# Kernel tuning notes

Measured on AMD Instinct MI355X. Metric: run time of the kernel, lower is better.

## Reference

```python
import jax, jax.numpy as jnp
import numpy as np

TAU = 0.001
TEMPERATURE = 0.1


def setup_inputs() -> dict:
    key = jax.random.key(0)
    k1, k2 = jax.random.split(key)
    B, H, N, L = 2, 8, 256, 64
    X = jax.random.normal(k1, (B, H, N, L), dtype=jnp.float32)
    Y = jax.random.normal(k2, (B, H, N, L), dtype=jnp.float32)
    return {"X": X, "Y": Y}


def _softsort_p2(scores):
    # scores: [B,H,N,L] -> s: [B,H,L,N]
    s = jnp.transpose(scores, (0, 1, 3, 2))
    srt = -jnp.sort(-s, axis=-1)  # descending sort along N
    # pairwise squared diff: rows = sorted values, cols = original values -> [B,H,L,N,N]
    pd = -((s[..., None, :] - srt[..., :, None]) ** 2) / TAU
    return jax.nn.softmax(pd, axis=-1)


def reference(X, Y):
    # Soft permutation matrices: [B,H,L,N,N]
    Pu = _softsort_p2(X)
    Pv = _softsort_p2(Y)
    # Gamma = Pu^T @ Pv  (contract over sorted-row index i)
    Gamma = jnp.einsum('bhlij,bhlik->bhljk', Pu, Pv)
    # cdist(X, Y, p=2) over last dim L -> [B,H,N,N]
    x2 = jnp.sum(X * X, axis=-1)            # [B,H,N]
    y2 = jnp.sum(Y * Y, axis=-1)            # [B,H,N]
    xy = jnp.einsum('bhnl,bhml->bhnm', X, Y)
    cost = jnp.sqrt(jnp.maximum(x2[..., :, None] + y2[..., None, :] - 2.0 * xy, 1e-12))
    # swds[b,h,l] = sum_{j,k} cost[b,h,j,k] * Gamma[b,h,l,j,k]
    swds = jnp.einsum('bhjk,bhljk->bhl', cost, Gamma)
    # exp(-T*(swds - min)) / sum == softmax(-T * swds) over L
    weights = jax.nn.softmax(-TEMPERATURE * swds, axis=-1)  # [B,H,L]
    # weighted sum over L -> [B,H,N,N]
    return jnp.einsum('bhljk,bhl->bhjk', Gamma, weights)
```

## Files before the change

kernel.cpp:

```cpp
#include <hip/hip_runtime.h>
#include <math.h>

#define TEMP    0.1f
#define CEXP    -1442.6950408889634f
#define SQRTC   37.98283767f
#define LOG2E   1.4426950408889634f


typedef __attribute__((ext_vector_type(8))) _Float16 half8;
typedef __attribute__((ext_vector_type(8))) short short8;
typedef __attribute__((ext_vector_type(4))) float f32x4;
typedef __attribute__((ext_vector_type(2))) unsigned int u32x2;

__device__ __forceinline__ float fexp2(float x) { return __builtin_amdgcn_exp2f(x); }

__device__ __forceinline__ half8 ldsh8(const unsigned short* p) {
  return __builtin_bit_cast(half8, *(const short8*)p);
}

__device__ __forceinline__ unsigned bf16r(float f) {
  unsigned u = __float_as_uint(f);
  return (u + 0x7FFFu + ((u >> 16) & 1u)) >> 16;
}

__device__ __forceinline__ int tswz(int row, int g) {
  return row * 32 + (((g + (row >> 1)) & 3) << 3);
}

__global__ __launch_bounds__(256) void prep_kernel(const float* __restrict__ X,
                                                   const float* __restrict__ Y,
                                                   float* __restrict__ cost,
                                                   float* __restrict__ nssu, float* __restrict__ lziu,
                                                   float* __restrict__ nssv, float* __restrict__ lziv) {
  __shared__ __align__(16) float smem[256];
  const int tid = threadIdx.x;
  if (blockIdx.x < 1024) {
    const int jq = blockIdx.x & 63, bh = blockIdx.x >> 6;
    const int j0 = jq * 4;
    smem[tid] = X[((size_t)bh*256 + j0 + (tid >> 6))*64 + (tid & 63)];
    __syncthreads();
    const float4* yp = (const float4*)(Y + ((size_t)bh*256 + tid)*64);
    float dot[4] = {0.f,0.f,0.f,0.f}, x2[4] = {0.f,0.f,0.f,0.f}, y2 = 0.f;
#pragma unroll
    for (int t = 0; t < 16; ++t) {
      float4 yv = yp[t];
      y2 += yv.x*yv.x + yv.y*yv.y + yv.z*yv.z + yv.w*yv.w;
#pragma unroll
      for (int r = 0; r < 4; ++r) {
        float4 xv = ((const float4*)(smem + r*64))[t];
        dot[r] += xv.x*yv.x + xv.y*yv.y + xv.z*yv.z + xv.w*yv.w;
        x2[r]  += xv.x*xv.x + xv.y*xv.y + xv.z*xv.z + xv.w*xv.w;
      }
    }
#pragma unroll
    for (int r = 0; r < 4; ++r) {
      float c = x2[r] + y2 - 2.f*dot[r];
      cost[((size_t)bh*256 + j0 + r)*256 + tid] = sqrtf(fmaxf(c, 1e-12f));
    }
  } else {
    const int idx = blockIdx.x - 1024;
    const int l = idx & 63, bh = (idx >> 6) & 15, uv = idx >> 10;
    const float* S = uv ? Y : X;
    float* so = uv ? nssv : nssu;
    float* zo = uv ? lziv : lziu;
    float v = S[((size_t)bh*256 + tid)*64 + l];
#pragma unroll
    for (int k = 2; k <= 256; k <<= 1) {
#pragma unroll
      for (int j = k >> 1; j > 0; j >>= 1) {
        float o;
        if (j >= 64) {
          smem[tid] = v; __syncthreads();
          o = smem[tid ^ j]; __syncthreads();
        } else {
          o = __shfl_xor(v, j, 64);
        }
        const bool up    = ((tid & k) == 0);
        const bool lower = ((tid & j) == 0);
        float mn = fminf(v, o), mx = fmaxf(v, o);
        v = (up == lower) ? mn : mx;
      }
    }
    smem[tid] = v; __syncthreads();
    const int jc = 255 - tid;
    const float sv = smem[jc];
    const int lo = jc > 48 ? jc - 48 : 0;
    const int hi = jc < 207 ? jc + 48 : 255;
    float z = 0.f;
    for (int jj = lo; jj <= hi; ++jj) { float d = smem[jj] - sv; z += fexp2(d*d*CEXP); }
    const int base = (bh*64 + l)*256 + tid;
    so[base] = -SQRTC * sv; zo[base] = -__log2f(z);
  }
}

__device__ __forceinline__ void stage_slab(int t, int ib, float usc, float vsc,
                                           const float* __restrict__ nssU, const float* __restrict__ lzU,
                                           const float* __restrict__ nssV, const float* __restrict__ lzV,
                                           unsigned short* __restrict__ EU,
                                           unsigned short* __restrict__ EV) {
  {
    const int r = t & 127, g = t >> 7;
    const int i0 = ib + (g << 3);
    float e[8];
#pragma unroll
    for (int ii = 0; ii < 8; ++ii) {
      float d = usc + nssU[i0 + ii];
      e[ii] = fexp2(fmaf(-d, d, lzU[i0 + ii]));
    }
    uint4 w;
    w.x = __builtin_bit_cast(unsigned, __builtin_amdgcn_cvt_pkrtz(e[0], e[1]));
    w.y = __builtin_bit_cast(unsigned, __builtin_amdgcn_cvt_pkrtz(e[2], e[3]));
    w.z = __builtin_bit_cast(unsigned, __builtin_amdgcn_cvt_pkrtz(e[4], e[5]));
    w.w = __builtin_bit_cast(unsigned, __builtin_amdgcn_cvt_pkrtz(e[6], e[7]));
    *(uint4*)&EU[tswz(r, g)] = w;
  }
  {
    const int r = t & 255;
    const int gp = (t >> 8) << 1;
#pragma unroll
    for (int gg = 0; gg < 2; ++gg) {
      const int i0 = ib + ((gp + gg) << 3);
      float e[8];
#pragma unroll
      for (int ii = 0; ii < 8; ++ii) {
        float d = vsc + nssV[i0 + ii];
        e[ii] = fexp2(fmaf(-d, d, lzV[i0 + ii]));
      }
      uint4 w;
      w.x = __builtin_bit_cast(unsigned, __builtin_amdgcn_cvt_pkrtz(e[0], e[1]));
      w.y = __builtin_bit_cast(unsigned, __builtin_amdgcn_cvt_pkrtz(e[2], e[3]));
      w.z = __builtin_bit_cast(unsigned, __builtin_amdgcn_cvt_pkrtz(e[4], e[5]));
      w.w = __builtin_bit_cast(unsigned, __builtin_amdgcn_cvt_pkrtz(e[6], e[7]));
      *(uint4*)&EV[tswz(r, gp + gg)] = w;
    }
  }
}

__global__ __launch_bounds__(512, 4) void pass1_kernel(
    const float* __restrict__ X, const float* __restrict__ Y,
    const float* __restrict__ cost,
    const float* __restrict__ nssu, const float* __restrict__ lziu,
    const float* __restrict__ nssv, const float* __restrict__ lziv,
    float* __restrict__ parts, u32x2* __restrict__ gamma) {
  const int sb = blockIdx.x, l = blockIdx.y, bh = blockIdx.z;
  const int j0 = sb * 128;
  const int tid = threadIdx.x, wave = tid >> 6, lane = tid & 63;
  const int wj = (wave & 1) * 64, wk = (wave >> 1) * 64;
  const int m = lane & 15, q = lane >> 4;
  const int inner = m*32 + (((q + (m >> 1)) & 3) << 3);

  __shared__ float nssU[256], lzU[256], nssV[256], lzV[256];
  __shared__ __align__(16) unsigned short EU0[128*32], EU1[128*32];
  __shared__ __align__(16) unsigned short EV0[256*32], EV1[256*32];
  __shared__ float red[8];

  const int lb = (bh*64 + l)*256;
  const float usc = SQRTC * X[((size_t)bh*256 + j0 + (tid & 127))*64 + l];
  const float vsc = SQRTC * Y[((size_t)bh*256 + (tid & 255))*64 + l];
  if (tid < 256) { nssU[tid] = nssu[lb + tid]; lzU[tid] = lziu[lb + tid]; }
  else { const int t2 = tid - 256; nssV[t2] = nssv[lb + t2]; lzV[t2] = lziv[lb + t2]; }

  f32x4 acc[16];
#pragma unroll
  for (int t = 0; t < 16; ++t) acc[t] = (f32x4){0.f, 0.f, 0.f, 0.f};

  __syncthreads();
  stage_slab(tid, 0, usc, vsc, nssU, lzU, nssV, lzV, EU0, EV0);
  __syncthreads();
#pragma unroll 1
  for (int s = 0; s < 8; ++s) {
    const unsigned short* EUc = (s & 1) ? EU1 : EU0;
    const unsigned short* EVc = (s & 1) ? EV1 : EV0;
    unsigned short* EUn = (s & 1) ? EU0 : EU1;
    unsigned short* EVn = (s & 1) ? EV0 : EV1;
    half8 A[4], B[4];
#pragma unroll
    for (int mt = 0; mt < 4; ++mt) A[mt] = ldsh8(&EUc[(wj + mt*16)*32 + inner]);
#pragma unroll
    for (int nt = 0; nt < 4; ++nt) B[nt] = ldsh8(&EVc[(wk + nt*16)*32 + inner]);
    if (s < 7)
      stage_slab(tid, (s+1)*32, usc, vsc, nssU, lzU, nssV, lzV, EUn, EVn);
#pragma unroll
    for (int mt = 0; mt < 4; ++mt)
#pragma unroll
      for (int nt = 0; nt < 4; ++nt)
        acc[mt*4+nt] = __builtin_amdgcn_mfma_f32_16x16x32_f16(A[mt], B[nt], acc[mt*4+nt], 0, 0, 0);
    __syncthreads();
  }

  const float* cb = cost + (size_t)bh * 65536;
  const int gbase = ((bh*2 + sb)*8 + wave) * 16;
  float part = 0.f;
#pragma unroll
  for (int mt = 0; mt < 4; ++mt) {
#pragma unroll
    for (int nt = 0; nt < 4; ++nt) {
      const int col  = wk + nt*16 + m;
      const int rowb = j0 + wj + mt*16 + q*4;
      f32x4 a = acc[mt*4 + nt];
      part += a.x*cb[(size_t)(rowb+0)*256 + col] + a.y*cb[(size_t)(rowb+1)*256 + col]
            + a.z*cb[(size_t)(rowb+2)*256 + col] + a.w*cb[(size_t)(rowb+3)*256 + col];
      u32x2 pk;
      pk.x = bf16r(a.x) | (bf16r(a.y) << 16);
      pk.y = bf16r(a.z) | (bf16r(a.w) << 16);
      gamma[((size_t)(gbase + mt*4 + nt)*64 + l)*64 + lane] = pk;
    }
  }
#pragma unroll
  for (int o = 32; o > 0; o >>= 1) part += __shfl_down(part, o, 64);
  if (lane == 0) red[wave] = part;
  __syncthreads();
  if (tid == 0) {
    float s8 = red[0]+red[1]+red[2]+red[3]+red[4]+red[5]+red[6]+red[7];
    parts[sb*1024 + bh*64 + l] = s8;
  }
}

__global__ __launch_bounds__(256) void wsum_kernel(const u32x2* __restrict__ g,
                                                   const float* __restrict__ parts,
                                                   float* __restrict__ out) {
  const int wv = threadIdx.x >> 6, lane = threadIdx.x & 63;
  const int bh = blockIdx.x >> 6;
  __shared__ float w[64];
  if (wv == 0) {
    float s = parts[bh*64 + lane] + parts[1024 + bh*64 + lane];
    float v = -TEMP * s * LOG2E;
    float mx = v;
#pragma unroll
    for (int o = 32; o > 0; o >>= 1) mx = fmaxf(mx, __shfl_xor(mx, o, 64));
    float e = fexp2(v - mx);
    float ssum = e;
#pragma unroll
    for (int o = 32; o > 0; o >>= 1) ssum += __shfl_xor(ssum, o, 64);
    w[lane] = e / ssum;
  }
  __syncthreads();
  const int group = blockIdx.x * 4 + wv;
  const u32x2* gp = g + (size_t)group*4096 + lane;
  float4 acc = {0.f, 0.f, 0.f, 0.f};
#pragma unroll 8
  for (int l = 0; l < 64; ++l) {
    u32x2 pk = gp[l*64];
    float wl = w[l];
    acc.x += wl * __uint_as_float(pk.x << 16);
    acc.y += wl * __uint_as_float(pk.x & 0xFFFF0000u);
    acc.z += wl * __uint_as_float(pk.y << 16);
    acc.w += wl * __uint_as_float(pk.y & 0xFFFF0000u);
  }
  const int frag = group & 15;
  const int idx  = group >> 4;
  const int wave = idx & 7, sbb = (idx >> 3) & 1;
  const int mt = frag >> 2, nt = frag & 3;
  const int m = lane & 15, q = lane >> 4;
  const int row = sbb*128 + (wave & 1)*64 + mt*16 + q*4;
  const int col = (wave >> 1)*64 + nt*16 + m;
  float* ob = out + ((size_t)bh*256 + row)*256 + col;
  __builtin_nontemporal_store(acc.x, &ob[0]);
  __builtin_nontemporal_store(acc.y, &ob[256]);
  __builtin_nontemporal_store(acc.z, &ob[512]);
  __builtin_nontemporal_store(acc.w, &ob[768]);
}

extern "C" void kernel_launch(void* const* d_in, const int* in_sizes, int n_in,
                              void* d_out, int out_size, void* d_ws, size_t ws_size,
                              hipStream_t stream) {
  (void)in_sizes; (void)n_in; (void)out_size; (void)ws_size;
  const float* X = (const float*)d_in[0];
  const float* Y = (const float*)d_in[1];
  float* out = (float*)d_out;
  float* ws  = (float*)d_ws;
  float* cost  = ws;
  float* nssu  = ws   + 1048576;
  float* lziu  = nssu + 262144;
  float* nssv  = lziu + 262144;
  float* lziv  = nssv + 262144;
  float* parts = lziv + 262144;
  u32x2* gamma = (u32x2*)(parts + 2048);

  prep_kernel <<<dim3(3072),      256, 0, stream>>>(X, Y, cost, nssu, lziu, nssv, lziv);
  pass1_kernel<<<dim3(2, 64, 16), 512, 0, stream>>>(X, Y, cost, nssu, lziu, nssv, lziv,
                                                    parts, gamma);
  wsum_kernel <<<dim3(1024),      256, 0, stream>>>(gamma, parts, out);
}
```

Before: 163.3 us.

## Fuse per-column sort and normalizer into pass1, vectorize LDS loads, split wsum over L

The bitonic sort and log-normalizer computation for each (bh,l) column moves from the prep kernel into pass1, which now computes them in shared memory (reusing the EU0 buffer). This removes 2048 prep blocks and the global round-trip of nss/lz arrays. The cost is that both sb blocks of a column redo the same sort. Stage_slab now reads nss/lz with float4 LDS loads. Wsum splits the L reduction across two waves per output group with an LDS combine, giving more blocks and shorter dependency chains.

Measured after the change: 181.6 us. 11.2% more time.

```diff
diff --git a/kernel.cpp b/kernel.cpp
--- a/kernel.cpp
+++ b/kernel.cpp
@@ -29,67 +29,30 @@
 
 __global__ __launch_bounds__(256) void prep_kernel(const float* __restrict__ X,
                                                    const float* __restrict__ Y,
-                                                   float* __restrict__ cost,
-                                                   float* __restrict__ nssu, float* __restrict__ lziu,
-                                                   float* __restrict__ nssv, float* __restrict__ lziv) {
+                                                   float* __restrict__ cost) {
   __shared__ __align__(16) float smem[256];
   const int tid = threadIdx.x;
-  if (blockIdx.x < 1024) {
-    const int jq = blockIdx.x & 63, bh = blockIdx.x >> 6;
-    const int j0 = jq * 4;
-    smem[tid] = X[((size_t)bh*256 + j0 + (tid >> 6))*64 + (tid & 63)];
-    __syncthreads();
-    const float4* yp = (const float4*)(Y + ((size_t)bh*256 + tid)*64);
-    float dot[4] = {0.f,0.f,0.f,0.f}, x2[4] = {0.f,0.f,0.f,0.f}, y2 = 0.f;
-#pragma unroll
-    for (int t = 0; t < 16; ++t) {
-      float4 yv = yp[t];
-      y2 += yv.x*yv.x + yv.y*yv.y + yv.z*yv.z + yv.w*yv.w;
-#pragma unroll
-      for (int r = 0; r < 4; ++r) {
-        float4 xv = ((const float4*)(smem + r*64))[t];
-        dot[r] += xv.x*yv.x + xv.y*yv.y + xv.z*yv.z + xv.w*yv.w;
-        x2[r]  += xv.x*xv.x + xv.y*xv.y + xv.z*xv.z + xv.w*xv.w;
-      }
-    }
+  const int jq = blockIdx.x & 63, bh = blockIdx.x >> 6;
+  const int j0 = jq * 4;
+  smem[tid] = X[((size_t)bh*256 + j0 + (tid >> 6))*64 + (tid & 63)];
+  __syncthreads();
+  const float4* yp = (const float4*)(Y + ((size_t)bh*256 + tid)*64);
+  float dot[4] = {0.f,0.f,0.f,0.f}, x2[4] = {0.f,0.f,0.f,0.f}, y2 = 0.f;
+#pragma unroll
+  for (int t = 0; t < 16; ++t) {
+    float4 yv = yp[t];
+    y2 += yv.x*yv.x + yv.y*yv.y + yv.z*yv.z + yv.w*yv.w;
 #pragma unroll
     for (int r = 0; r < 4; ++r) {
-      float c = x2[r] + y2 - 2.f*dot[r];
-      cost[((size_t)bh*256 + j0 + r)*256 + tid] = sqrtf(fmaxf(c, 1e-12f));
-    }
-  } else {
-    const int idx = blockIdx.x - 1024;
-    const int l = idx & 63, bh = (idx >> 6) & 15, uv = idx >> 10;
-    const float* S = uv ? Y : X;
-    float* so = uv ? nssv : nssu;
-    float* zo = uv ? lziv : lziu;
-    float v = S[((size_t)bh*256 + tid)*64 + l];
-#pragma unroll
-    for (int k = 2; k <= 256; k <<= 1) {
-#pragma unroll
-      for (int j = k >> 1; j > 0; j >>= 1) {
-        float o;
-        if (j >= 64) {
-          smem[tid] = v; __syncthreads();
-          o = smem[tid ^ j]; __syncthreads();
-        } else {
-          o = __shfl_xor(v, j, 64);
-        }
-        const bool up    = ((tid & k) == 0);
-        const bool lower = ((tid & j) == 0);
-        float mn = fminf(v, o), mx = fmaxf(v, o);
-        v = (up == lower) ? mn : mx;
-      }
-    }
-    smem[tid] = v; __syncthreads();
-    const int jc = 255 - tid;
-    const float sv = smem[jc];
-    const int lo = jc > 48 ? jc - 48 : 0;
-    const int hi = jc < 207 ? jc + 48 : 255;
-    float z = 0.f;
-    for (int jj = lo; jj <= hi; ++jj) { float d = smem[jj] - sv; z += fexp2(d*d*CEXP); }
-    const int base = (bh*64 + l)*256 + tid;
-    so[base] = -SQRTC * sv; zo[base] = -__log2f(z);
+      float4 xv = ((const float4*)(smem + r*64))[t];
+      dot[r] += xv.x*yv.x + xv.y*yv.y + xv.z*yv.z + xv.w*yv.w;
+      x2[r]  += xv.x*xv.x + xv.y*xv.y + xv.z*xv.z + xv.w*xv.w;
+    }
+  }
+#pragma unroll
+  for (int r = 0; r < 4; ++r) {
+    float c = x2[r] + y2 - 2.f*dot[r];
+    cost[((size_t)bh*256 + j0 + r)*256 + tid] = sqrtf(fmaxf(c, 1e-12f));
   }
 }
 
@@ -101,12 +64,17 @@
   {
     const int r = t & 127, g = t >> 7;
     const int i0 = ib + (g << 3);
-    float e[8];
-#pragma unroll
-    for (int ii = 0; ii < 8; ++ii) {
-      float d = usc + nssU[i0 + ii];
-      e[ii] = fexp2(fmaf(-d, d, lzU[i0 + ii]));
-    }
+    float4 n0 = *(const float4*)&nssU[i0], n1 = *(const float4*)&nssU[i0+4];
+    float4 z0 = *(const float4*)&lzU[i0],  z1 = *(const float4*)&lzU[i0+4];
+    float e[8], d;
+    d = usc + n0.x; e[0] = fexp2(fmaf(-d, d, z0.x));
+    d = usc + n0.y; e[1] = fexp2(fmaf(-d, d, z0.y));
+    d = usc + n0.z; e[2] = fexp2(fmaf(-d, d, z0.z));
+    d = usc + n0.w; e[3] = fexp2(fmaf(-d, d, z0.w));
+    d = usc + n1.x; e[4] = fexp2(fmaf(-d, d, z1.x));
+    d = usc + n1.y; e[5] = fexp2(fmaf(-d, d, z1.y));
+    d = usc + n1.z; e[6] = fexp2(fmaf(-d, d, z1.z));
+    d = usc + n1.w; e[7] = fexp2(fmaf(-d, d, z1.w));
     uint4 w;
     w.x = __builtin_bit_cast(unsigned, __builtin_amdgcn_cvt_pkrtz(e[0], e[1]));
     w.y = __builtin_bit_cast(unsigned, __builtin_amdgcn_cvt_pkrtz(e[2], e[3]));
@@ -120,12 +88,17 @@
 #pragma unroll
     for (int gg = 0; gg < 2; ++gg) {
       const int i0 = ib + ((gp + gg) << 3);
-      float e[8];
-#pragma unroll
-      for (int ii = 0; ii < 8; ++ii) {
-        float d = vsc + nssV[i0 + ii];
-        e[ii] = fexp2(fmaf(-d, d, lzV[i0 + ii]));
-      }
+      float4 n0 = *(const float4*)&nssV[i0], n1 = *(const float4*)&nssV[i0+4];
+      float4 z0 = *(const float4*)&lzV[i0],  z1 = *(const float4*)&lzV[i0+4];
+      float e[8], d;
+      d = vsc + n0.x; e[0] = fexp2(fmaf(-d, d, z0.x));
+      d = vsc + n0.y; e[1] = fexp2(fmaf(-d, d, z0.y));
+      d = vsc + n0.z; e[2] = fexp2(fmaf(-d, d, z0.z));
+      d = vsc + n0.w; e[3] = fexp2(fmaf(-d, d, z0.w));
+      d = vsc + n1.x; e[4] = fexp2(fmaf(-d, d, z1.x));
+      d = vsc + n1.y; e[5] = fexp2(fmaf(-d, d, z1.y));
+      d = vsc + n1.z; e[6] = fexp2(fmaf(-d, d, z1.z));
+      d = vsc + n1.w; e[7] = fexp2(fmaf(-d, d, z1.w));
       uint4 w;
       w.x = __builtin_bit_cast(unsigned, __builtin_amdgcn_cvt_pkrtz(e[0], e[1]));
       w.y = __builtin_bit_cast(unsigned, __builtin_amdgcn_cvt_pkrtz(e[2], e[3]));
@@ -139,8 +112,6 @@
 __global__ __launch_bounds__(512, 4) void pass1_kernel(
     const float* __restrict__ X, const float* __restrict__ Y,
     const float* __restrict__ cost,
-    const float* __restrict__ nssu, const float* __restrict__ lziu,
-    const float* __restrict__ nssv, const float* __restrict__ lziv,
     float* __restrict__ parts, u32x2* __restrict__ gamma) {
   const int sb = blockIdx.x, l = blockIdx.y, bh = blockIdx.z;
   const int j0 = sb * 128;
@@ -149,22 +120,56 @@
   const int m = lane & 15, q = lane >> 4;
   const int inner = m*32 + (((q + (m >> 1)) & 3) << 3);
 
-  __shared__ float nssU[256], lzU[256], nssV[256], lzV[256];
+  __shared__ __align__(16) float nssU[256], lzU[256], nssV[256], lzV[256];
   __shared__ __align__(16) unsigned short EU0[128*32], EU1[128*32];
   __shared__ __align__(16) unsigned short EV0[256*32], EV1[256*32];
   __shared__ float red[8];
 
-  const int lb = (bh*64 + l)*256;
   const float usc = SQRTC * X[((size_t)bh*256 + j0 + (tid & 127))*64 + l];
   const float vsc = SQRTC * Y[((size_t)bh*256 + (tid & 255))*64 + l];
-  if (tid < 256) { nssU[tid] = nssu[lb + tid]; lzU[tid] = lziu[lb + tid]; }
-  else { const int t2 = tid - 256; nssV[t2] = nssv[lb + t2]; lzV[t2] = lziv[lb + t2]; }
+
+  {
+    float* sb2 = (float*)EU0;
+    const int half = tid >> 8, t = tid & 255;
+    float* s = sb2 + half*256;
+    const float* S = half ? Y : X;
+    float v = S[((size_t)bh*256 + t)*64 + l];
+#pragma unroll
+    for (int k = 2; k <= 256; k <<= 1) {
+#pragma unroll
+      for (int j = k >> 1; j > 0; j >>= 1) {
+        float o;
+        if (j >= 64) {
+          s[t] = v; __syncthreads();
+          o = s[t ^ j]; __syncthreads();
+        } else {
+          o = __shfl_xor(v, j, 64);
+        }
+        const bool up  = ((t & k) == 0);
+        const bool low = ((t & j) == 0);
+        float mn = fminf(v, o), mx = fmaxf(v, o);
+        v = (up == low) ? mn : mx;
+      }
+    }
+    s[t] = v;
+    __syncthreads();
+    const int jc = 255 - t;
+    const float sv = s[jc];
+    const int lo = jc > 48 ? jc - 48 : 0;
+    const int hi = jc < 207 ? jc + 48 : 255;
+    float z = 0.f;
+    for (int jj = lo; jj <= hi; ++jj) { float d = s[jj] - sv; z += fexp2(d*d*CEXP); }
+    float* nss = half ? nssV : nssU;
+    float* lz  = half ? lzV  : lzU;
+    nss[t] = -SQRTC * sv;
+    lz[t]  = -__log2f(z);
+  }
+  __syncthreads();
 
   f32x4 acc[16];
 #pragma unroll
   for (int t = 0; t < 16; ++t) acc[t] = (f32x4){0.f, 0.f, 0.f, 0.f};
 
-  __syncthreads();
   stage_slab(tid, 0, usc, vsc, nssU, lzU, nssV, lzV, EU0, EV0);
   __syncthreads();
 #pragma unroll 1
@@ -216,13 +221,15 @@
   }
 }
 
-__global__ __launch_bounds__(256) void wsum_kernel(const u32x2* __restrict__ g,
+__global__ __launch_bounds__(128) void wsum_kernel(const u32x2* __restrict__ g,
                                                    const float* __restrict__ parts,
                                                    float* __restrict__ out) {
   const int wv = threadIdx.x >> 6, lane = threadIdx.x & 63;
-  const int bh = blockIdx.x >> 6;
+  const int group = blockIdx.x;
+  const int bh = group >> 8;
   __shared__ float w[64];
-  if (wv == 0) {
+  __shared__ __align__(16) float psum[256];
+  if (threadIdx.x < 64) {
     float s = parts[bh*64 + lane] + parts[1024 + bh*64 + lane];
     float v = -TEMP * s * LOG2E;
     float mx = v;
@@ -235,30 +242,35 @@
     w[lane] = e / ssum;
   }
   __syncthreads();
-  const int group = blockIdx.x * 4 + wv;
-  const u32x2* gp = g + (size_t)group*4096 + lane;
+  const u32x2* gp = g + (size_t)group*4096 + (size_t)(wv*32)*64 + lane;
   float4 acc = {0.f, 0.f, 0.f, 0.f};
 #pragma unroll 8
-  for (int l = 0; l < 64; ++l) {
+  for (int l = 0; l < 32; ++l) {
     u32x2 pk = gp[l*64];
-    float wl = w[l];
+    float wl = w[wv*32 + l];
     acc.x += wl * __uint_as_float(pk.x << 16);
     acc.y += wl * __uint_as_float(pk.x & 0xFFFF0000u);
     acc.z += wl * __uint_as_float(pk.y << 16);
     acc.w += wl * __uint_as_float(pk.y & 0xFFFF0000u);
   }
-  const int frag = group & 15;
-  const int idx  = group >> 4;
-  const int wave = idx & 7, sbb = (idx >> 3) & 1;
-  const int mt = frag >> 2, nt = frag & 3;
-  const int m = lane & 15, q = lane >> 4;
-  const int row = sbb*128 + (wave & 1)*64 + mt*16 + q*4;
-  const int col = (wave >> 1)*64 + nt*16 + m;
-  float* ob = out + ((size_t)bh*256 + row)*256 + col;
-  __builtin_nontemporal_store(acc.x, &ob[0]);
-  __builtin_nontemporal_store(acc.y, &ob[256]);
-  __builtin_nontemporal_store(acc.z, &ob[512]);
-  __builtin_nontemporal_store(acc.w, &ob[768]);
+  if (wv == 1) *(float4*)&psum[lane*4] = acc;
+  __syncthreads();
+  if (wv == 0) {
+    float4 o2 = *(const float4*)&psum[lane*4];
+    acc.x += o2.x; acc.y += o2.y; acc.z += o2.z; acc.w += o2.w;
+    const int frag = group & 15;
+    const int idx  = group >> 4;
+    const int wave = idx & 7, sbb = (idx >> 3) & 1;
+    const int mt = frag >> 2, nt = frag & 3;
+    const int m = lane & 15, q = lane >> 4;
+    const int row = sbb*128 + (wave & 1)*64 + mt*16 + q*4;
+    const int col = (wave >> 1)*64 + nt*16 + m;
+    float* ob = out + ((size_t)bh*256 + row)*256 + col;
+    __builtin_nontemporal_store(acc.x, &ob[0]);
+    __builtin_nontemporal_store(acc.y, &ob[256]);
+    __builtin_nontemporal_store(acc.z, &ob[512]);
+    __builtin_nontemporal_store(acc.w, &ob[768]);
+  }
 }
 
 extern "C" void kernel_launch(void* const* d_in, const int* in_sizes, int n_in,
@@ -270,15 +282,10 @@
   float* out = (float*)d_out;
   float* ws  = (float*)d_ws;
   float* cost  = ws;
-  float* nssu  = ws   + 1048576;
-  float* lziu  = nssu + 262144;
-  float* nssv  = lziu + 262144;
-  float* lziv  = nssv + 262144;
-  float* parts = lziv + 262144;
+  float* parts = ws + 1048576;
   u32x2* gamma = (u32x2*)(parts + 2048);
 
-  prep_kernel <<<dim3(3072),      256, 0, stream>>>(X, Y, cost, nssu, lziu, nssv, lziv);
-  pass1_kernel<<<dim3(2, 64, 16), 512, 0, stream>>>(X, Y, cost, nssu, lziu, nssv, lziv,
-                                                    parts, gamma);
-  wsum_kernel <<<dim3(1024),      256, 0, stream>>>(gamma, parts, out);
-}
+  prep_kernel <<<dim3(1024),      256, 0, stream>>>(X, Y, cost);
+  pass1_kernel<<<dim3(2, 64, 16), 512, 0, stream>>>(X, Y, cost, parts, gamma);
+  wsum_kernel <<<dim3(4096),      128, 0, stream>>>(gamma, parts, out);
+}
```
